# Kernel optimization log

Hardware: AMD Instinct MI355X
Metric: run time of the kernel (lower is better)

## Reference

```python
import jax, jax.numpy as jnp
import numpy as np

NUM_HEADS = 8

def setup_inputs() -> dict:
    key = jax.random.key(0)
    ks = jax.random.split(key, 4)
    A, B, H, QD = 256, 256, 2048, 2048
    xav = (6.0 / (H + H)) ** 0.5  # xavier_uniform bound for square weights
    return {
        "q": jax.random.normal(ks[0], (A, B, H), dtype=jnp.float32),
        "k": jax.random.normal(ks[1], (B, QD), dtype=jnp.float32),
        "Wq": jax.random.uniform(ks[2], (H, H), dtype=jnp.float32, minval=-xav, maxval=xav),
        "bq": jnp.zeros((H,), dtype=jnp.float32),
        "Wk": jax.random.uniform(ks[3], (H, QD), dtype=jnp.float32, minval=-xav, maxval=xav),
        "bk": jnp.zeros((H,), dtype=jnp.float32),
    }


def reference(q, k, Wq, bq, Wk, bk):
    n = NUM_HEADS
    H = Wq.shape[0]
    c = H // n
    fact = (H / n) ** -0.5
    # Linear projections (the dominant GEMMs)
    ql = jnp.einsum('abh,oh->abo', q, Wq) + bq          # [A, B, H]
    kl = jnp.einsum('bd,od->bo', k, Wk) + bk            # [B, H]
    A, B, _ = ql.shape
    # permute(1,2,0) then reshape (scrambling reshape, faithful to torch C-order)
    qp = jnp.transpose(ql, (1, 2, 0))                   # [B, H, A]
    qh = qp.reshape(A, B, n, c)                         # [A, B, n, c]
    # k: permute(1,0) -> [H, B], unsqueeze twice -> [H, B, 1, 1], reshape
    kp = jnp.transpose(kl)[:, :, None, None]            # [H, B, 1, 1]
    kh = kp.reshape(B, n, c, 1, 1)                      # [B(q-axis), n, c, 1, 1]
    # attention map einsum; h=w=1 here
    w = jnp.einsum('bqnc,qnchw->bqnhw', qh * fact, kh)  # [A, B, n, 1, 1]
    # softmax over flattened (n*h*w) dims
    w = jax.nn.softmax(w.reshape(A, B, -1), axis=-1).reshape(w.shape)
    return w
```

## Files before the change

kernel.cpp:

```cpp
#include <hip/hip_runtime.h>
#include <stdint.h>


typedef __attribute__((ext_vector_type(8))) __bf16 bf16x8;
typedef __attribute__((ext_vector_type(4))) __bf16 bf16x4;
typedef __attribute__((ext_vector_type(4))) float f32x4;

__device__ __forceinline__ void gload_lds16(const void* g, void* l) {
  __builtin_amdgcn_global_load_lds(
      (const __attribute__((address_space(1))) uint32_t*)g,
      (__attribute__((address_space(3))) uint32_t*)l, 16, 0, 0);
}

__global__ void convert_kernel(const float* __restrict__ qin,
                               const float* __restrict__ Wq,
                               const float* __restrict__ Wk,
                               const float* __restrict__ kin,
                               void* __restrict__ q_t,
                               void* __restrict__ wq_b, void* __restrict__ wk_b,
                               void* __restrict__ k_b) {
  const int NQ0 = 33554432;
  const int NQ1 = 1048576;
  const int NQ2 = 1048576;
  const int NQ3 = 131072;
  const int TOT = NQ0 + NQ1 + NQ2 + NQ3;
  for (int i = blockIdx.x * blockDim.x + threadIdx.x; i < TOT;
       i += gridDim.x * blockDim.x) {
    if (i < NQ0) {
      float4 v = ((const float4*)qin)[i];
      const int jq = i & 511;
      const int b  = (i >> 9) & 255;
      const int c  = i >> 17;
      bf16x4 o;
      o[0] = (__bf16)v.x; o[1] = (__bf16)v.y; o[2] = (__bf16)v.z; o[3] = (__bf16)v.w;
      ((bf16x4*)q_t)[(int64_t)(((b << 8) + c) << 9) + jq] = o;
    } else {
      const float4* src; bf16x4* dst; int j;
      if (i < NQ0+NQ1)              { src = (const float4*)Wq;  dst = (bf16x4*)wq_b; j = i - NQ0; }
      else if (i < NQ0+NQ1+NQ2)     { src = (const float4*)Wk;  dst = (bf16x4*)wk_b; j = i - NQ0 - NQ1; }
      else                          { src = (const float4*)kin; dst = (bf16x4*)k_b;  j = i - NQ0 - NQ1 - NQ2; }
      float4 v = src[j];
      bf16x4 o;
      o[0] = (__bf16)v.x; o[1] = (__bf16)v.y; o[2] = (__bf16)v.z; o[3] = (__bf16)v.w;
      dst[j] = o;
    }
  }
}

__global__ __launch_bounds__(256)
void kl_kernel(const void* __restrict__ k_b, const void* __restrict__ wk_b,
               const float* __restrict__ bk, void* __restrict__ kl_t_v) {
  __shared__ char smem[32768];
  const __bf16* kb   = (const __bf16*)k_b;
  const __bf16* wkb  = (const __bf16*)wk_b;
  __bf16* kl_t = (__bf16*)kl_t_v;
  const int t = threadIdx.x, w = t >> 6, l = t & 63;
  const int ntile = blockIdx.x, mtile = blockIdx.y;
  const int wr = w >> 1, wc = w & 1;
  f32x4 acc[2][2] = {};

  auto stage = [&](int buf, int kt) {
    const int row = t >> 3;
    const int col = (((t & 7) ^ (row & 7)) << 3);
#pragma unroll
    for (int i = 0; i < 2; ++i) {
      const __bf16* ga = kb + (int64_t)(mtile*64 + i*32 + row) * 2048 + kt*64 + col;
      gload_lds16(ga, smem + buf*16384 + (i*256 + w*64)*16);
      const __bf16* gb = wkb + (int64_t)(ntile*64 + i*32 + row) * 2048 + kt*64 + col;
      gload_lds16(gb, smem + buf*16384 + 8192 + (i*256 + w*64)*16);
    }
  };

  stage(0, 0);
  __syncthreads();
  int cur = 0;
  for (int kt = 0; kt < 32; ++kt) {
    if (kt + 1 < 32) stage(cur ^ 1, kt + 1);
    const char* bA = smem + cur*16384;
    const char* bB = smem + cur*16384 + 8192;
#pragma unroll
    for (int kq = 0; kq < 2; ++kq) {
      bf16x8 a[2], b[2];
      const int g = kq*4 + (l >> 4);
#pragma unroll
      for (int mi = 0; mi < 2; ++mi) {
        const int r = wr*32 + mi*16 + (l & 15);
        a[mi] = *(const bf16x8*)(bA + r*128 + ((g ^ (r & 7)) << 4));
      }
#pragma unroll
      for (int ni = 0; ni < 2; ++ni) {
        const int r = wc*32 + ni*16 + (l & 15);
        b[ni] = *(const bf16x8*)(bB + r*128 + ((g ^ (r & 7)) << 4));
      }
#pragma unroll
      for (int mi = 0; mi < 2; ++mi)
#pragma unroll
        for (int ni = 0; ni < 2; ++ni)
          acc[mi][ni] = __builtin_amdgcn_mfma_f32_16x16x32_bf16(a[mi], b[ni], acc[mi][ni], 0, 0, 0);
    }
    __syncthreads();
    cur ^= 1;
  }

#pragma unroll
  for (int ni = 0; ni < 2; ++ni) {
    const int o = ntile*64 + wc*32 + ni*16 + (l & 15);
    const float bko = bk[o];
#pragma unroll
    for (int mi = 0; mi < 2; ++mi) {
      const int c0 = mtile*64 + wr*32 + mi*16 + (l >> 4)*4;
      bf16x4 v;
      v[0] = (__bf16)(acc[mi][ni][0] + bko);
      v[1] = (__bf16)(acc[mi][ni][1] + bko);
      v[2] = (__bf16)(acc[mi][ni][2] + bko);
      v[3] = (__bf16)(acc[mi][ni][3] + bko);
      *(bf16x4*)(kl_t + (int64_t)o*256 + c0) = v;
    }
  }
}

#define PHASE(BUF, QM, QN, STAGE_STMT, VM_STMT) do {                          \
  const char* bA_ = smem + (BUF)*32768;                                       \
  const char* bB_ = smem + 65536 + (BUF)*32768;                               \
  bf16x8 afx0[4], afx1[4], bfx0[2], bfx1[2];                                  \
  {                                                                           \
    const int lg_ = l >> 4;                                                   \
    _Pragma("unroll") for (int j2 = 0; j2 < 4; ++j2) {                        \
      const int r_ = wr*128 + ((QM)*4 + j2)*16 + (l & 15);                    \
      afx0[j2] = *(const bf16x8*)(bA_ + r_*128 + ((lg_ ^ (r_ & 7)) << 4));    \
      afx1[j2] = *(const bf16x8*)(bA_ + r_*128 + (((4+lg_) ^ (r_ & 7)) << 4));\
    }                                                                         \
    _Pragma("unroll") for (int n2 = 0; n2 < 2; ++n2) {                        \
      const int r_ = wc*64 + ((QN)*2 + n2)*16 + (l & 15);                     \
      bfx0[n2] = *(const bf16x8*)(bB_ + r_*128 + ((lg_ ^ (r_ & 7)) << 4));    \
      bfx1[n2] = *(const bf16x8*)(bB_ + r_*128 + (((4+lg_) ^ (r_ & 7)) << 4));\
    }                                                                         \
  }                                                                           \
  STAGE_STMT;                                                                 \
  asm volatile("s_waitcnt lgkmcnt(8)" ::: "memory");                          \
  __builtin_amdgcn_s_barrier();                                               \
  asm volatile("s_waitcnt lgkmcnt(0)" ::: "memory");                          \
  __builtin_amdgcn_sched_barrier(0);                                          \
  __builtin_amdgcn_s_setprio(1);                                              \
  _Pragma("unroll") for (int j2 = 0; j2 < 4; ++j2)                            \
    _Pragma("unroll") for (int n2 = 0; n2 < 2; ++n2)                          \
      acc[(QM)*4+j2][(QN)*2+n2] = __builtin_amdgcn_mfma_f32_16x16x32_bf16(    \
          afx0[j2], bfx0[n2], acc[(QM)*4+j2][(QN)*2+n2], 0, 0, 0);            \
  _Pragma("unroll") for (int j2 = 0; j2 < 4; ++j2)                            \
    _Pragma("unroll") for (int n2 = 0; n2 < 2; ++n2)                          \
      acc[(QM)*4+j2][(QN)*2+n2] = __builtin_amdgcn_mfma_f32_16x16x32_bf16(    \
          afx1[j2], bfx1[n2], acc[(QM)*4+j2][(QN)*2+n2], 0, 0, 0);            \
  __builtin_amdgcn_s_setprio(0);                                              \
  VM_STMT;                                                                    \
  __builtin_amdgcn_s_barrier();                                               \
} while (0)

__global__ __launch_bounds__(512, 2)
void main_kernel(const void* __restrict__ q_tv, const void* __restrict__ wq_b,
                 const float* __restrict__ bq, const void* __restrict__ kl_t_v,
                 float* __restrict__ out) {
  __shared__ char smem[131072];
  const __bf16* qt   = (const __bf16*)q_tv;
  const __bf16* wqb  = (const __bf16*)wq_b;
  const __bf16* kl_t = (const __bf16*)kl_t_v;
  const int t = threadIdx.x, w = t >> 6, l = t & 63;
  const int otile = blockIdx.x, b = blockIdx.y;
  const int wr = w >> 2, wc = w & 3;
  f32x4 acc[8][4] = {};

  auto stageA = [&](int buf, int kt, int qm) {
#pragma unroll
    for (int i = 0; i < 2; ++i) {
      const int r = i*128 + qm*64 + (t >> 3);
      const int sg = (t & 7) ^ (r & 7);
      const __bf16* ga = qt + (int64_t)(b*256 + r) * 2048 + kt*64 + sg*8;
      gload_lds16(ga, smem + buf*32768 + r*128 + (t & 7)*16);
    }
  };
  auto stageB = [&](int buf, int kt, int qn) {
#pragma unroll
    for (int i = 0; i < 2; ++i) {
      const int row64 = t >> 3;
      const int r = i*128 + qn*32 + (row64 & 31) + ((row64 >> 5) << 6);
      const int sg = (t & 7) ^ (r & 7);
      const __bf16* gb = wqb + (int64_t)(otile*256 + r) * 2048 + kt*64 + sg*8;
      gload_lds16(gb, smem + 65536 + buf*32768 + r*128 + (t & 7)*16);
    }
  };

  stageA(0, 0, 0); stageA(0, 0, 1); stageB(0, 0, 0); stageB(0, 0, 1);
  stageA(1, 1, 0); stageB(1, 1, 0);
  asm volatile("s_waitcnt vmcnt(4)" ::: "memory");
  __builtin_amdgcn_s_barrier();

  for (int j = 0; j < 16; ++j) {
    const int kt0 = 2*j, kt1 = 2*j + 1;
    const bool p2 = (j < 15);
    PHASE(0, 0, 0, { stageA(1, kt1, 1); }, {});
    PHASE(0, 0, 1, { stageB(1, kt1, 1); }, {});
    PHASE(0, 1, 0, { if (p2) stageA(0, kt0+2, 0); }, {});
    PHASE(0, 1, 1, { if (p2) stageB(0, kt0+2, 0); },
          { if (p2) { asm volatile("s_waitcnt vmcnt(4)" ::: "memory"); }
            else    { asm volatile("s_waitcnt vmcnt(0)" ::: "memory"); } });
    PHASE(1, 0, 0, { if (p2) stageA(0, kt0+2, 1); }, {});
    PHASE(1, 0, 1, { if (p2) stageB(0, kt0+2, 1); }, {});
    PHASE(1, 1, 0, { if (p2) stageA(1, kt1+2, 0); }, {});
    PHASE(1, 1, 1, { if (p2) stageB(1, kt1+2, 0); },
          { if (p2) { asm volatile("s_waitcnt vmcnt(4)" ::: "memory"); } });
  }

  float psum[4] = {0.f, 0.f, 0.f, 0.f};
#pragma unroll
  for (int ni = 0; ni < 4; ++ni) {
    const int o = otile*256 + wc*64 + ni*16 + (l & 15);
    const float bqo = bq[o];
    const __bf16* klc = kl_t + (int64_t)o * 256 + wr*128 + (l >> 4)*4;
#pragma unroll
    for (int mi = 0; mi < 8; ++mi) {
      bf16x4 kv = *(const bf16x4*)(klc + mi*16);
      psum[ni] += (acc[mi][ni][0] + bqo) * (float)kv[0]
                + (acc[mi][ni][1] + bqo) * (float)kv[1]
                + (acc[mi][ni][2] + bqo) * (float)kv[2]
                + (acc[mi][ni][3] + bqo) * (float)kv[3];
    }
  }
#pragma unroll
  for (int ni = 0; ni < 4; ++ni) {
    psum[ni] += __shfl_xor(psum[ni], 16);
    psum[ni] += __shfl_xor(psum[ni], 32);
  }
  float* red = (float*)smem;
  if (l < 16) {
#pragma unroll
    for (int ni = 0; ni < 4; ++ni)
      red[wr*256 + wc*64 + ni*16 + l] = psum[ni];
  }
  __syncthreads();
  if (t < 256) {
    const float s = 0.0625f * (red[t] + red[256 + t]);
    float m = s;
    m = fmaxf(m, __shfl_xor(m, 1));
    m = fmaxf(m, __shfl_xor(m, 2));
    m = fmaxf(m, __shfl_xor(m, 4));
    const float e = __expf(s - m);
    float sum = e;
    sum += __shfl_xor(sum, 1);
    sum += __shfl_xor(sum, 2);
    sum += __shfl_xor(sum, 4);
    out[(int64_t)b*2048 + otile*256 + t] = e / sum;
  }
}

extern "C" void kernel_launch(void* const* d_in, const int* in_sizes, int n_in,
                              void* d_out, int out_size, void* d_ws, size_t ws_size,
                              hipStream_t stream) {
  (void)in_sizes; (void)n_in; (void)out_size; (void)ws_size;
  const float* q  = (const float*)d_in[0];
  const float* k  = (const float*)d_in[1];
  const float* Wq = (const float*)d_in[2];
  const float* bq = (const float*)d_in[3];
  const float* Wk = (const float*)d_in[4];
  const float* bk = (const float*)d_in[5];
  float* out = (float*)d_out;
  char* ws = (char*)d_ws;
  void* q_t  = ws;
  void* wq_b = ws + 268435456;
  void* wk_b = ws + 268435456 + 8388608;
  void* k_b  = ws + 268435456 + 16777216;
  void* kl_t = ws + 268435456 + 17825792;

  convert_kernel<<<2048, 256, 0, stream>>>(q, Wq, Wk, k, q_t, wq_b, wk_b, k_b);
  kl_kernel<<<dim3(32, 4), 256, 0, stream>>>(k_b, wk_b, bk, kl_t);
  main_kernel<<<dim3(8, 256), 512, 0, stream>>>(q_t, wq_b, bq, kl_t, out);
}
```

Measured before the change: 710.9 us.

## Triple-buffer A tiles and halve barrier phases per k-step in GEMM pipeline

The main GEMM loop moves from four quadrant phases per k-tile to two phases per k-tile, each covering a full 32-wide K half with all 8x4 MFMAs. A tiles are now triple-buffered and prefetched two k-tiles ahead, while B tiles stay double-buffered and are prefetched one tile ahead. LDS grows from 128KB to 160KB. The aim is fewer barriers and better overlap of global-to-LDS loads with MFMA work. The cost is more LDS per block and more complex wait-count bookkeeping.

Result: faster. 673.5 us (-5.3%).

```diff
diff --git a/kernel.cpp b/kernel.cpp
--- a/kernel.cpp
+++ b/kernel.cpp
@@ -119,21 +119,19 @@
   }
 }
 
-#define PHASE(BUF, QM, QN, STAGE_STMT, VM_STMT) do {                          \
-  const char* bA_ = smem + (BUF)*32768;                                       \
-  const char* bB_ = smem + 65536 + (BUF)*32768;                               \
-  bf16x8 afx0[4], afx1[4], bfx0[2], bfx1[2];                                  \
+#define PHASE2(ABUF, BBUF, H, STAGE_STMT, VM_STMT) do {                       \
+  const char* bA_ = smem + (ABUF)*32768;                                      \
+  const char* bB_ = smem + 98304 + (BBUF)*32768;                              \
+  bf16x8 af[8]; bf16x8 bf[4];                                                 \
   {                                                                           \
-    const int lg_ = l >> 4;                                                   \
-    _Pragma("unroll") for (int j2 = 0; j2 < 4; ++j2) {                        \
-      const int r_ = wr*128 + ((QM)*4 + j2)*16 + (l & 15);                    \
-      afx0[j2] = *(const bf16x8*)(bA_ + r_*128 + ((lg_ ^ (r_ & 7)) << 4));    \
-      afx1[j2] = *(const bf16x8*)(bA_ + r_*128 + (((4+lg_) ^ (r_ & 7)) << 4));\
+    const int g_ = (H)*4 + (l >> 4);                                          \
+    _Pragma("unroll") for (int m2 = 0; m2 < 8; ++m2) {                        \
+      const int r_ = wr*128 + m2*16 + (l & 15);                               \
+      af[m2] = *(const bf16x8*)(bA_ + r_*128 + ((g_ ^ (r_ & 7)) << 4));       \
     }                                                                         \
-    _Pragma("unroll") for (int n2 = 0; n2 < 2; ++n2) {                        \
-      const int r_ = wc*64 + ((QN)*2 + n2)*16 + (l & 15);                     \
-      bfx0[n2] = *(const bf16x8*)(bB_ + r_*128 + ((lg_ ^ (r_ & 7)) << 4));    \
-      bfx1[n2] = *(const bf16x8*)(bB_ + r_*128 + (((4+lg_) ^ (r_ & 7)) << 4));\
+    _Pragma("unroll") for (int n2 = 0; n2 < 4; ++n2) {                        \
+      const int r_ = wc*64 + n2*16 + (l & 15);                                \
+      bf[n2] = *(const bf16x8*)(bB_ + r_*128 + ((g_ ^ (r_ & 7)) << 4));       \
     }                                                                         \
   }                                                                           \
   STAGE_STMT;                                                                 \
@@ -142,14 +140,10 @@
   asm volatile("s_waitcnt lgkmcnt(0)" ::: "memory");                          \
   __builtin_amdgcn_sched_barrier(0);                                          \
   __builtin_amdgcn_s_setprio(1);                                              \
-  _Pragma("unroll") for (int j2 = 0; j2 < 4; ++j2)                            \
-    _Pragma("unroll") for (int n2 = 0; n2 < 2; ++n2)                          \
-      acc[(QM)*4+j2][(QN)*2+n2] = __builtin_amdgcn_mfma_f32_16x16x32_bf16(    \
-          afx0[j2], bfx0[n2], acc[(QM)*4+j2][(QN)*2+n2], 0, 0, 0);            \
-  _Pragma("unroll") for (int j2 = 0; j2 < 4; ++j2)                            \
-    _Pragma("unroll") for (int n2 = 0; n2 < 2; ++n2)                          \
-      acc[(QM)*4+j2][(QN)*2+n2] = __builtin_amdgcn_mfma_f32_16x16x32_bf16(    \
-          afx1[j2], bfx1[n2], acc[(QM)*4+j2][(QN)*2+n2], 0, 0, 0);            \
+  _Pragma("unroll") for (int m2 = 0; m2 < 8; ++m2)                            \
+    _Pragma("unroll") for (int n2 = 0; n2 < 4; ++n2)                          \
+      acc[m2][n2] = __builtin_amdgcn_mfma_f32_16x16x32_bf16(                  \
+          af[m2], bf[n2], acc[m2][n2], 0, 0, 0);                              \
   __builtin_amdgcn_s_setprio(0);                                              \
   VM_STMT;                                                                    \
   __builtin_amdgcn_s_barrier();                                               \
@@ -159,7 +153,7 @@
 void main_kernel(const void* __restrict__ q_tv, const void* __restrict__ wq_b,
                  const float* __restrict__ bq, const void* __restrict__ kl_t_v,
                  float* __restrict__ out) {
-  __shared__ char smem[131072];
+  __shared__ char smem[163840];
   const __bf16* qt   = (const __bf16*)q_tv;
   const __bf16* wqb  = (const __bf16*)wq_b;
   const __bf16* kl_t = (const __bf16*)kl_t_v;
@@ -168,45 +162,45 @@
   const int wr = w >> 2, wc = w & 3;
   f32x4 acc[8][4] = {};
 
-  auto stageA = [&](int buf, int kt, int qm) {
+  auto stageA = [&](int buf, int kt, int half) {
 #pragma unroll
     for (int i = 0; i < 2; ++i) {
-      const int r = i*128 + qm*64 + (t >> 3);
+      const int r = i*128 + half*64 + (t >> 3);
       const int sg = (t & 7) ^ (r & 7);
       const __bf16* ga = qt + (int64_t)(b*256 + r) * 2048 + kt*64 + sg*8;
       gload_lds16(ga, smem + buf*32768 + r*128 + (t & 7)*16);
     }
   };
-  auto stageB = [&](int buf, int kt, int qn) {
+  auto stageB = [&](int buf, int kt, int half) {
 #pragma unroll
     for (int i = 0; i < 2; ++i) {
       const int row64 = t >> 3;
-      const int r = i*128 + qn*32 + (row64 & 31) + ((row64 >> 5) << 6);
+      const int r = i*128 + half*32 + (row64 & 31) + ((row64 >> 5) << 6);
       const int sg = (t & 7) ^ (r & 7);
       const __bf16* gb = wqb + (int64_t)(otile*256 + r) * 2048 + kt*64 + sg*8;
-      gload_lds16(gb, smem + 65536 + buf*32768 + r*128 + (t & 7)*16);
+      gload_lds16(gb, smem + 98304 + buf*32768 + r*128 + (t & 7)*16);
     }
   };
 
-  stageA(0, 0, 0); stageA(0, 0, 1); stageB(0, 0, 0); stageB(0, 0, 1);
-  stageA(1, 1, 0); stageB(1, 1, 0);
+  stageA(0, 0, 0); stageA(0, 0, 1);
+  stageB(0, 0, 0); stageB(0, 0, 1);
+  stageA(1, 1, 0); stageA(1, 1, 1);
   asm volatile("s_waitcnt vmcnt(4)" ::: "memory");
   __builtin_amdgcn_s_barrier();
 
-  for (int j = 0; j < 16; ++j) {
-    const int kt0 = 2*j, kt1 = 2*j + 1;
-    const bool p2 = (j < 15);
-    PHASE(0, 0, 0, { stageA(1, kt1, 1); }, {});
-    PHASE(0, 0, 1, { stageB(1, kt1, 1); }, {});
-    PHASE(0, 1, 0, { if (p2) stageA(0, kt0+2, 0); }, {});
-    PHASE(0, 1, 1, { if (p2) stageB(0, kt0+2, 0); },
-          { if (p2) { asm volatile("s_waitcnt vmcnt(4)" ::: "memory"); }
-            else    { asm volatile("s_waitcnt vmcnt(0)" ::: "memory"); } });
-    PHASE(1, 0, 0, { if (p2) stageA(0, kt0+2, 1); }, {});
-    PHASE(1, 0, 1, { if (p2) stageB(0, kt0+2, 1); }, {});
-    PHASE(1, 1, 0, { if (p2) stageA(1, kt1+2, 0); }, {});
-    PHASE(1, 1, 1, { if (p2) stageB(1, kt1+2, 0); },
-          { if (p2) { asm volatile("s_waitcnt vmcnt(4)" ::: "memory"); } });
+  int ac = 0;
+  for (int kt = 0; kt < 32; ++kt) {
+    const int as = (ac >= 1) ? ac - 1 : ac + 2;
+    const int bc = kt & 1, bs = bc ^ 1;
+    const bool sA = (kt < 30), sB = (kt < 31);
+    PHASE2(ac, bc, 0,
+           { if (sB) { stageB(bs, kt + 1, 0); stageB(bs, kt + 1, 1); } },
+           {});
+    PHASE2(ac, bc, 1,
+           { if (sA) { stageA(as, kt + 2, 0); stageA(as, kt + 2, 1); } },
+           { if (sA)      { asm volatile("s_waitcnt vmcnt(4)" ::: "memory"); }
+             else if (sB) { asm volatile("s_waitcnt vmcnt(0)" ::: "memory"); } });
+    ac = (ac == 2) ? 0 : ac + 1;
   }
 
   float psum[4] = {0.f, 0.f, 0.f, 0.f};
```
